# Performance work log

Hardware: AMD Instinct MI355X
Metric: run time of the kernel (lower is better)

Reference implementation:

```python
import jax, jax.numpy as jnp
import numpy as np

B, C, G = 2, 256, 32
SPATIAL = (16, 16, 16)
EPS = 1e-5


def setup_inputs() -> dict:
    key = jax.random.key(0)
    ks = jax.random.split(key, 11)
    s = 1.0 / np.sqrt(C)
    x = jax.random.normal(ks[0], (B, C) + SPATIAL, dtype=jnp.float32)
    mk = lambda k: jax.random.normal(k, (C, C), dtype=jnp.float32) * s
    return {
        "x": x,
        "Wq": mk(ks[1]), "bq": jnp.zeros((C,), jnp.float32),
        "Wk": mk(ks[2]), "bk": jnp.zeros((C,), jnp.float32),
        "Wv": mk(ks[3]), "bv": jnp.zeros((C,), jnp.float32),
        "Wo": mk(ks[4]), "bo": jnp.zeros((C,), jnp.float32),
        "gamma": jnp.ones((C,), jnp.float32),
        "beta": jnp.zeros((C,), jnp.float32),
    }


def reference(x, Wq, bq, Wk, bk, Wv, bv, Wo, bo, gamma, beta):
    b, c = x.shape[0], x.shape[1]
    xf = x.reshape(b, c, -1)  # [B, C, N]

    def proj1x1(inp, W, bias):
        return jnp.einsum('oc,bcn->bon', W, inp) + bias[None, :, None]

    q = proj1x1(xf, Wq, bq)
    k = proj1x1(xf, Wk, bk)
    v = proj1x1(xf, Wv, bv)

    # qk[b, n, m] = sum_c q[b, c, n] * k[b, c, m]   (no 1/sqrt(C) scale, as in source)
    scores = jnp.einsum('bcn,bcm->bnm', q, k)
    w = jax.nn.softmax(scores, axis=-1)
    # h[b, c, n] = sum_m v[b, c, m] * w[b, n, m]
    h = jnp.einsum('bcm,bnm->bcn', v, w)
    h = proj1x1(h, Wo, bo)

    y = xf + h  # residual

    # GroupNorm over (channels-in-group, spatial)
    yg = y.reshape(b, G, c // G, -1)
    mu = jnp.mean(yg, axis=(2, 3), keepdims=True)
    var = jnp.var(yg, axis=(2, 3), keepdims=True)
    yn = ((yg - mu) * jax.lax.rsqrt(var + EPS)).reshape(b, c, -1)
    yn = yn * gamma[None, :, None] + beta[None, :, None]

    out = yn * jax.nn.sigmoid(yn)  # SiLU
    return out.reshape(x.shape)
```

## Files before the change

kernel.cpp:

```cpp
#include <hip/hip_runtime.h>
#include <hip/hip_bf16.h>

typedef _Float16 f16;
typedef __attribute__((ext_vector_type(4))) _Float16 f16x4;
typedef __attribute__((ext_vector_type(8))) _Float16 f16x8;
typedef __attribute__((ext_vector_type(4))) float f32x4;

#define CD 256
#define ND 4096
#define GD 32
#define KVB 32

__device__ __forceinline__ void gl_lds16(const f16* g, f16* l) {
    __builtin_amdgcn_global_load_lds(
        (const __attribute__((address_space(1))) unsigned int*)g,
        (__attribute__((address_space(3))) unsigned int*)l,
        16, 0, 0);
}

__global__ __launch_bounds__(256)
void k_proj_qkv(const float* __restrict__ x,
                const float* __restrict__ Wq, const float* __restrict__ bq,
                const float* __restrict__ Wk, const float* __restrict__ bk,
                const float* __restrict__ Wv, const float* __restrict__ bv,
                f16* __restrict__ Qt, f16* __restrict__ Kt, f16* __restrict__ Vb)
{
    __shared__ f16 As[64][40];
    __shared__ f16 Bs[64][40];
    __shared__ f16 Ts[64][72];

    const int t  = threadIdx.x;
    const int n0 = blockIdx.x * 64;
    const int o0 = blockIdx.y * 64;
    const int p  = blockIdx.z % 3;
    const int bb = blockIdx.z / 3;

    const float* W    = (p == 0) ? Wq : (p == 1) ? Wk : Wv;
    const float* bias = (p == 0) ? bq : (p == 1) ? bk : bv;

    const int w  = t >> 6;
    const int l  = t & 63;
    const int lr = l & 15;
    const int lg = l >> 4;
    const int wo = (w >> 1) * 32;
    const int wn = (w & 1) * 32;

    const int sl = t & 63;
    const int k8 = (t >> 6) * 8;

    f32x4 acc[2][2] = {};

    for (int ck = 0; ck < CD; ck += 32) {
        __syncthreads();
        {
            const float* s = W + (size_t)(o0 + sl) * CD + ck + k8;
            f16x8 v;
#pragma unroll
            for (int u = 0; u < 8; ++u) v[u] = (f16)s[u];
            *(f16x8*)&As[sl][k8] = v;
        }
        {
            const float* s = x + ((size_t)bb * CD + ck + k8) * ND + n0 + sl;
            f16x8 v;
#pragma unroll
            for (int u = 0; u < 8; ++u) v[u] = (f16)s[(size_t)u * ND];
            *(f16x8*)&Bs[sl][k8] = v;
        }
        __syncthreads();
        f16x8 a0 = *(const f16x8*)&As[wo + lr][lg * 8];
        f16x8 a1 = *(const f16x8*)&As[wo + 16 + lr][lg * 8];
        f16x8 b0 = *(const f16x8*)&Bs[wn + lr][lg * 8];
        f16x8 b1 = *(const f16x8*)&Bs[wn + 16 + lr][lg * 8];
        acc[0][0] = __builtin_amdgcn_mfma_f32_16x16x32_f16(a0, b0, acc[0][0], 0, 0, 0);
        acc[0][1] = __builtin_amdgcn_mfma_f32_16x16x32_f16(a0, b1, acc[0][1], 0, 0, 0);
        acc[1][0] = __builtin_amdgcn_mfma_f32_16x16x32_f16(a1, b0, acc[1][0], 0, 0, 0);
        acc[1][1] = __builtin_amdgcn_mfma_f32_16x16x32_f16(a1, b1, acc[1][1], 0, 0, 0);
    }

    if (p < 2) {
        __syncthreads();
#pragma unroll
        for (int so = 0; so < 2; ++so)
#pragma unroll
            for (int r = 0; r < 4; ++r) {
                int orow  = wo + so * 16 + lg * 4 + r;
                float bv_ = bias[o0 + orow];
#pragma unroll
                for (int sn = 0; sn < 2; ++sn)
                    Ts[orow][wn + sn * 16 + lr] = (f16)(acc[so][sn][r] + bv_);
            }
        __syncthreads();
        f16* dst = (p == 0) ? Qt : Kt;
        int n  = t >> 2;
        int o8 = (t & 3) * 16;
        f16 tmp[16];
#pragma unroll
        for (int u = 0; u < 16; ++u) tmp[u] = Ts[o8 + u][n];
        f16* g = dst + ((size_t)bb * ND + n0 + n) * CD + o0 + o8;
        *(f16x8*)g       = *(f16x8*)&tmp[0];
        *(f16x8*)(g + 8) = *(f16x8*)&tmp[8];
    } else {
#pragma unroll
        for (int so = 0; so < 2; ++so)
#pragma unroll
            for (int r = 0; r < 4; ++r) {
                int orow  = wo + so * 16 + lg * 4 + r;
                float bv_ = bias[o0 + orow];
#pragma unroll
                for (int sn = 0; sn < 2; ++sn) {
                    int ncol = wn + sn * 16 + lr;
                    Vb[((size_t)bb * CD + o0 + orow) * ND + n0 + ncol] =
                        (f16)(acc[so][sn][r] + bv_);
                }
            }
    }
}

template<int KSN>
__global__ __launch_bounds__(256, 2)
void k_attn(const f16* __restrict__ Qt, const f16* __restrict__ Kt,
            const f16* __restrict__ Vb, f16* __restrict__ Op,
            float* __restrict__ ml)
{
    __shared__ f16 Ks[2][32 * 256];
    __shared__ f16 Vs[2][256 * 32];
    __shared__ f16 Pl[4][32][40];

    const int t  = threadIdx.x;
    const int w  = t >> 6;
    const int l  = t & 63;
    const int lr = l & 15;
    const int lg = l >> 4;
    const int ks = blockIdx.y;
    const int bb = blockIdx.z;
    const int q0 = blockIdx.x * 128 + w * 32;

    f16x8 qf[2][8];
#pragma unroll
    for (int qs = 0; qs < 2; ++qs)
#pragma unroll
        for (int kc = 0; kc < 8; ++kc)
            qf[qs][kc] = *(const f16x8*)(Qt + ((size_t)bb * ND + q0 + qs * 16 + lr) * CD + kc * 32 + lg * 8);

    f32x4 oacc[2][16] = {};
    float row_m[2] = { -3.0e38f, -3.0e38f };
    float row_l[2] = { 0.f, 0.f };

    const int kv0 = ks * (ND / KSN);
    const f16* ktb = Kt + (size_t)bb * ND * CD;
    const f16* vbb = Vb + (size_t)bb * CD * ND;

    int koff[4], voff[4];
#pragma unroll
    for (int j = 0; j < 4; ++j) {
        int v   = (w * 4 + j) * 64 + l;
        int row = v >> 5;
        int ch  = (v & 31) ^ (row & 7);
        koff[j] = row * CD + ch * 8;
        int c   = v >> 2;
        int u   = (v & 3) ^ ((c >> 1) & 3);
        voff[j] = c * ND + u * 8;
    }

    auto stage = [&](int m0, int bi) {
#pragma unroll
        for (int j = 0; j < 4; ++j)
            gl_lds16(ktb + (size_t)m0 * CD + koff[j], &Ks[bi][(w * 4 + j) * 512]);
#pragma unroll
        for (int j = 0; j < 4; ++j)
            gl_lds16(vbb + m0 + voff[j], &Vs[bi][(w * 4 + j) * 512]);
    };

    stage(kv0, 0);
    __syncthreads();

    const int NIT = (ND / KSN) / KVB;
    for (int it = 0; it < NIT; ++it) {
        const int bi = it & 1;
        if (it + 1 < NIT) stage(kv0 + (it + 1) * KVB, bi ^ 1);

        f32x4 s[2][2] = {};
        __builtin_amdgcn_s_setprio(1);
#pragma unroll
        for (int kc = 0; kc < 8; ++kc) {
            int chs = ((kc * 4 + lg) ^ (lr & 7)) * 8;
            f16x8 k0 = *(const f16x8*)&Ks[bi][(lr) * 256 + chs];
            f16x8 k1 = *(const f16x8*)&Ks[bi][(16 + lr) * 256 + chs];
            s[0][0] = __builtin_amdgcn_mfma_f32_16x16x32_f16(k0, qf[0][kc], s[0][0], 0, 0, 0);
            s[1][0] = __builtin_amdgcn_mfma_f32_16x16x32_f16(k1, qf[0][kc], s[1][0], 0, 0, 0);
            s[0][1] = __builtin_amdgcn_mfma_f32_16x16x32_f16(k0, qf[1][kc], s[0][1], 0, 0, 0);
            s[1][1] = __builtin_amdgcn_mfma_f32_16x16x32_f16(k1, qf[1][kc], s[1][1], 0, 0, 0);
        }
        __builtin_amdgcn_s_setprio(0);

#pragma unroll
        for (int qs = 0; qs < 2; ++qs) {
            float pm = fmaxf(
                fmaxf(fmaxf(s[0][qs][0], s[0][qs][1]), fmaxf(s[0][qs][2], s[0][qs][3])),
                fmaxf(fmaxf(s[1][qs][0], s[1][qs][1]), fmaxf(s[1][qs][2], s[1][qs][3])));
            pm = fmaxf(pm, __shfl_xor(pm, 16));
            pm = fmaxf(pm, __shfl_xor(pm, 32));
            float nm = fmaxf(row_m[qs], pm);
            float sc = __expf(row_m[qs] - nm);
            float p0 = __expf(s[0][qs][0] - nm);
            float p1 = __expf(s[0][qs][1] - nm);
            float p2 = __expf(s[0][qs][2] - nm);
            float p3 = __expf(s[0][qs][3] - nm);
            float p4 = __expf(s[1][qs][0] - nm);
            float p5 = __expf(s[1][qs][1] - nm);
            float p6 = __expf(s[1][qs][2] - nm);
            float p7 = __expf(s[1][qs][3] - nm);
            float ps = ((p0 + p1) + (p2 + p3)) + ((p4 + p5) + (p6 + p7));
            ps += __shfl_xor(ps, 16);
            ps += __shfl_xor(ps, 32);
            bool chg = nm > row_m[qs];
            row_l[qs] = row_l[qs] * sc + ps;
            row_m[qs] = nm;
            if (__any(chg)) {
#pragma unroll
                for (int ct = 0; ct < 16; ++ct) {
                    oacc[qs][ct][0] *= sc; oacc[qs][ct][1] *= sc;
                    oacc[qs][ct][2] *= sc; oacc[qs][ct][3] *= sc;
                }
            }
            f16x4 pk0 = { (f16)p0, (f16)p1, (f16)p2, (f16)p3 };
            f16x4 pk1 = { (f16)p4, (f16)p5, (f16)p6, (f16)p7 };
            *(f16x4*)&Pl[w][qs * 16 + lr][lg * 4]      = pk0;
            *(f16x4*)&Pl[w][qs * 16 + lr][16 + lg * 4] = pk1;
        }

        f16x8 pf0 = *(const f16x8*)&Pl[w][lr][lg * 8];
        f16x8 pf1 = *(const f16x8*)&Pl[w][16 + lr][lg * 8];
        __builtin_amdgcn_s_setprio(1);
#pragma unroll
        for (int ct = 0; ct < 16; ++ct) {
            f16x8 vf = *(const f16x8*)&Vs[bi][(ct * 16 + lr) * 32 + ((lg ^ ((lr >> 1) & 3))) * 8];
            oacc[0][ct] = __builtin_amdgcn_mfma_f32_16x16x32_f16(vf, pf0, oacc[0][ct], 0, 0, 0);
            oacc[1][ct] = __builtin_amdgcn_mfma_f32_16x16x32_f16(vf, pf1, oacc[1][ct], 0, 0, 0);
        }
        __builtin_amdgcn_s_setprio(0);
        __syncthreads();
    }

#pragma unroll
    for (int qs = 0; qs < 2; ++qs)
#pragma unroll
        for (int ct = 0; ct < 16; ++ct)
#pragma unroll
            for (int r = 0; r < 4; ++r) {
                int cch = ct * 16 + lg * 4 + r;
                Op[(((size_t)ks * 2 + bb) * CD + cch) * ND + q0 + qs * 16 + lr] =
                    (f16)oacc[qs][ct][r];
            }
    if (lg == 0) {
#pragma unroll
        for (int qs = 0; qs < 2; ++qs) {
            int n = q0 + qs * 16 + lr;
            ml[((ks * 2 + bb) * 2 + 0) * ND + n] = row_m[qs];
            ml[((ks * 2 + bb) * 2 + 1) * ND + n] = row_l[qs];
        }
    }
}

template<int KSN>
__global__ __launch_bounds__(256)
void k_ml(const float* __restrict__ ml, float* __restrict__ wq)
{
    int i = blockIdx.x * 256 + threadIdx.x;
    int b = i / ND, n = i % ND;
    float m[KSN], lv[KSN];
#pragma unroll
    for (int ks = 0; ks < KSN; ++ks) {
        m[ks]  = ml[((ks * 2 + b) * 2 + 0) * ND + n];
        lv[ks] = ml[((ks * 2 + b) * 2 + 1) * ND + n];
    }
    float M = m[0];
#pragma unroll
    for (int ks = 1; ks < KSN; ++ks) M = fmaxf(M, m[ks]);
    float wgt[KSN], L = 0.f;
#pragma unroll
    for (int ks = 0; ks < KSN; ++ks) { wgt[ks] = __expf(m[ks] - M); L += wgt[ks] * lv[ks]; }
    float inv = 1.0f / L;
#pragma unroll
    for (int ks = 0; ks < KSN; ++ks)
        wq[(ks * 2 + b) * ND + n] = wgt[ks] * inv;
}

template<int KSN>
__global__ __launch_bounds__(256)
void k_comb(const f16* __restrict__ Op, const float* __restrict__ wq,
            f16* __restrict__ Hb)
{
    size_t i = (size_t)blockIdx.x * 256 + threadIdx.x;
    int n0 = (int)(i % (ND / 8)) * 8;
    int c  = (int)((i / (ND / 8)) % CD);
    int b  = (int)(i / ((size_t)CD * (ND / 8)));

    float acc[8] = {};
#pragma unroll
    for (int ks = 0; ks < KSN; ++ks) {
        f16x8 o = *(const f16x8*)(Op + (((size_t)ks * 2 + b) * CD + c) * ND + n0);
        const float* wp = wq + (ks * 2 + b) * ND + n0;
        float4 w0 = *(const float4*)wp;
        float4 w1 = *(const float4*)(wp + 4);
        acc[0] += w0.x * (float)o[0]; acc[1] += w0.y * (float)o[1];
        acc[2] += w0.z * (float)o[2]; acc[3] += w0.w * (float)o[3];
        acc[4] += w1.x * (float)o[4]; acc[5] += w1.y * (float)o[5];
        acc[6] += w1.z * (float)o[6]; acc[7] += w1.w * (float)o[7];
    }
    f16x8 h;
#pragma unroll
    for (int u = 0; u < 8; ++u) h[u] = (f16)acc[u];
    *(f16x8*)(Hb + ((size_t)b * CD + c) * ND + n0) = h;
}

__global__ __launch_bounds__(256)
void k_proj_o(const f16* __restrict__ Hb, const float* __restrict__ Wo,
              const float* __restrict__ bo, const float* __restrict__ x,
              float* __restrict__ Y)
{
    __shared__ f16 As[64][40];
    __shared__ f16 Bs[64][40];

    const int t  = threadIdx.x;
    const int n0 = blockIdx.x * 64;
    const int o0 = blockIdx.y * 64;
    const int bb = blockIdx.z;

    const int w  = t >> 6;
    const int l  = t & 63;
    const int lr = l & 15;
    const int lg = l >> 4;
    const int wo = (w >> 1) * 32;
    const int wn = (w & 1) * 32;

    const int sl = t & 63;
    const int k8 = (t >> 6) * 8;

    f32x4 acc[2][2] = {};

    for (int ck = 0; ck < CD; ck += 32) {
        __syncthreads();
        {
            const float* s = Wo + (size_t)(o0 + sl) * CD + ck + k8;
            f16x8 v;
#pragma unroll
            for (int u = 0; u < 8; ++u) v[u] = (f16)s[u];
            *(f16x8*)&As[sl][k8] = v;
        }
        {
            const f16* s = Hb + ((size_t)bb * CD + ck + k8) * ND + n0 + sl;
            f16x8 v;
#pragma unroll
            for (int u = 0; u < 8; ++u) v[u] = s[(size_t)u * ND];
            *(f16x8*)&Bs[sl][k8] = v;
        }
        __syncthreads();
        f16x8 a0 = *(const f16x8*)&As[wo + lr][lg * 8];
        f16x8 a1 = *(const f16x8*)&As[wo + 16 + lr][lg * 8];
        f16x8 b0 = *(const f16x8*)&Bs[wn + lr][lg * 8];
        f16x8 b1 = *(const f16x8*)&Bs[wn + 16 + lr][lg * 8];
        acc[0][0] = __builtin_amdgcn_mfma_f32_16x16x32_f16(a0, b0, acc[0][0], 0, 0, 0);
        acc[0][1] = __builtin_amdgcn_mfma_f32_16x16x32_f16(a0, b1, acc[0][1], 0, 0, 0);
        acc[1][0] = __builtin_amdgcn_mfma_f32_16x16x32_f16(a1, b0, acc[1][0], 0, 0, 0);
        acc[1][1] = __builtin_amdgcn_mfma_f32_16x16x32_f16(a1, b1, acc[1][1], 0, 0, 0);
    }

#pragma unroll
    for (int so = 0; so < 2; ++so)
#pragma unroll
        for (int r = 0; r < 4; ++r) {
            int orow  = wo + so * 16 + lg * 4 + r;
            float bv_ = bo[o0 + orow];
#pragma unroll
            for (int sn = 0; sn < 2; ++sn) {
                int ncol   = wn + sn * 16 + lr;
                size_t idx = ((size_t)bb * CD + o0 + orow) * ND + n0 + ncol;
                Y[idx] = acc[so][sn][r] + bv_ + x[idx];
            }
        }
}

__global__ __launch_bounds__(256)
void k_stats(const float* __restrict__ Y, float* __restrict__ stats)
{
    const int g = blockIdx.x, b = blockIdx.y;
    const float* base = Y + ((size_t)b * CD + g * 8) * ND;
    float s = 0.f, s2 = 0.f;
    for (int i = threadIdx.x; i < (8 * ND) / 4; i += 256) {
        float4 v = ((const float4*)base)[i];
        s  += v.x + v.y + v.z + v.w;
        s2 += v.x * v.x + v.y * v.y + v.z * v.z + v.w * v.w;
    }
#pragma unroll
    for (int m = 1; m < 64; m <<= 1) {
        s  += __shfl_xor(s, m);
        s2 += __shfl_xor(s2, m);
    }
    __shared__ float red[8];
    if ((threadIdx.x & 63) == 0) {
        red[(threadIdx.x >> 6) * 2]     = s;
        red[(threadIdx.x >> 6) * 2 + 1] = s2;
    }
    __syncthreads();
    if (threadIdx.x == 0) {
        float S  = red[0] + red[2] + red[4] + red[6];
        float S2 = red[1] + red[3] + red[5] + red[7];
        float mean = S / 32768.f;
        float var  = S2 / 32768.f - mean * mean;
        stats[(b * GD + g) * 2]     = mean;
        stats[(b * GD + g) * 2 + 1] = rsqrtf(var + 1e-5f);
    }
}

__global__ __launch_bounds__(256)
void k_norm_silu(const float* __restrict__ Y, const float* __restrict__ stats,
                 const float* __restrict__ gamma, const float* __restrict__ beta,
                 float* __restrict__ out)
{
    size_t i4 = (size_t)blockIdx.x * 256 + threadIdx.x;
    int c = (int)((i4 / (ND / 4)) % CD);
    int b = (int)(i4 / ((size_t)CD * (ND / 4)));
    float mean = stats[(b * GD + c / 8) * 2];
    float rstd = stats[(b * GD + c / 8) * 2 + 1];
    float ga = gamma[c], be = beta[c];
    float4 v = ((const float4*)Y)[i4];
    float in[4] = { v.x, v.y, v.z, v.w };
    float ob[4];
#pragma unroll
    for (int u = 0; u < 4; ++u) {
        float yn = (in[u] - mean) * rstd * ga + be;
        float sg = 1.0f / (1.0f + __expf(-yn));
        ob[u] = yn * sg;
    }
    *(float4*)(out + i4 * 4) = *(float4*)ob;
}

extern "C" void kernel_launch(void* const* d_in, const int* in_sizes, int n_in,
                              void* d_out, int out_size, void* d_ws, size_t ws_size,
                              hipStream_t stream)
{
    const float* x     = (const float*)d_in[0];
    const float* Wq    = (const float*)d_in[1];
    const float* bq    = (const float*)d_in[2];
    const float* Wk    = (const float*)d_in[3];
    const float* bk    = (const float*)d_in[4];
    const float* Wv    = (const float*)d_in[5];
    const float* bv    = (const float*)d_in[6];
    const float* Wo    = (const float*)d_in[7];
    const float* bo    = (const float*)d_in[8];
    const float* gamma = (const float*)d_in[9];
    const float* beta  = (const float*)d_in[10];

    char* ws = (char*)d_ws;
    f16* Qt = (f16*)(ws);
    f16* Kt = (f16*)(ws + (4u << 20));
    f16* Vb = (f16*)(ws + (8u << 20));
    f16* Hb = (f16*)(ws + (12u << 20));
    f16* Op = (f16*)(ws + (16u << 20));
    float* Y = (float*)(ws + (16u << 20));

    const bool big = ws_size >= (50ull << 20);

    k_proj_qkv<<<dim3(64, 4, 6), 256, 0, stream>>>(x, Wq, bq, Wk, bk, Wv, bv, Qt, Kt, Vb);

    if (big) {
        constexpr int KSN = 8;
        float* ml    = (float*)(ws + (48u << 20));
        float* wq    = (float*)(ws + (48u << 20) + (768u << 10));
        float* stats = (float*)(ws + (49u << 20) + (512u << 10));
        k_attn<KSN><<<dim3(32, KSN, 2), 256, 0, stream>>>(Qt, Kt, Vb, Op, ml);
        k_ml<KSN><<<dim3((2 * ND) / 256), 256, 0, stream>>>(ml, wq);
        k_comb<KSN><<<dim3((2 * CD * ND / 8) / 256), 256, 0, stream>>>(Op, wq, Hb);
        k_proj_o<<<dim3(64, 4, 2), 256, 0, stream>>>(Hb, Wo, bo, x, Y);
        k_stats<<<dim3(32, 2), 256, 0, stream>>>(Y, stats);
        k_norm_silu<<<2048, 256, 0, stream>>>(Y, stats, gamma, beta, (float*)d_out);
    } else {
        constexpr int KSN = 4;
        float* ml    = (float*)(ws + (32u << 20));
        float* wq    = (float*)(ws + (32u << 20) + (512u << 10));
        float* stats = (float*)(ws + (33u << 20));
        k_attn<KSN><<<dim3(32, KSN, 2), 256, 0, stream>>>(Qt, Kt, Vb, Op, ml);
        k_ml<KSN><<<dim3((2 * ND) / 256), 256, 0, stream>>>(ml, wq);
        k_comb<KSN><<<dim3((2 * CD * ND / 8) / 256), 256, 0, stream>>>(Op, wq, Hb);
        k_proj_o<<<dim3(64, 4, 2), 256, 0, stream>>>(Hb, Wo, bo, x, Y);
        k_stats<<<dim3(32, 2), 256, 0, stream>>>(Y, stats);
        k_norm_silu<<<2048, 256, 0, stream>>>(Y, stats, gamma, beta, (float*)d_out);
    }
}
```

Measured before the change: 121.3 us.

## Fuse QKV projections per block and split attention into 8 waves of 16 rows

The QKV projection kernel now computes Q, K and V in one block, sharing the x tile staged in LDS, instead of launching separate blocks per projection. The attention kernel moves to 512 threads, with each wave owning 16 query rows instead of 32. This halves the per-wave accumulator and Q-fragment registers and raises the occupancy target to 4 blocks. The trade-off is lower MFMA reuse of each K/V fragment per wave, more LDS traffic per FLOP, and fewer projection blocks with more registers each.

```diff
diff --git a/kernel.cpp b/kernel.cpp
--- a/kernel.cpp
+++ b/kernel.cpp
@@ -25,18 +25,17 @@
                 const float* __restrict__ Wv, const float* __restrict__ bv,
                 f16* __restrict__ Qt, f16* __restrict__ Kt, f16* __restrict__ Vb)
 {
-    __shared__ f16 As[64][40];
+    __shared__ f16 As[3][64][40];
     __shared__ f16 Bs[64][40];
     __shared__ f16 Ts[64][72];
 
     const int t  = threadIdx.x;
     const int n0 = blockIdx.x * 64;
     const int o0 = blockIdx.y * 64;
-    const int p  = blockIdx.z % 3;
-    const int bb = blockIdx.z / 3;
-
-    const float* W    = (p == 0) ? Wq : (p == 1) ? Wk : Wv;
-    const float* bias = (p == 0) ? bq : (p == 1) ? bk : bv;
+    const int bb = blockIdx.z;
+
+    const float* Ws[3] = { Wq, Wk, Wv };
+    const float* bs[3] = { bq, bk, bv };
 
     const int w  = t >> 6;
     const int l  = t & 63;
@@ -48,16 +47,17 @@
     const int sl = t & 63;
     const int k8 = (t >> 6) * 8;
 
-    f32x4 acc[2][2] = {};
+    f32x4 acc[3][2][2] = {};
 
     for (int ck = 0; ck < CD; ck += 32) {
         __syncthreads();
-        {
-            const float* s = W + (size_t)(o0 + sl) * CD + ck + k8;
+#pragma unroll
+        for (int p = 0; p < 3; ++p) {
+            const float* s = Ws[p] + (size_t)(o0 + sl) * CD + ck + k8;
             f16x8 v;
 #pragma unroll
             for (int u = 0; u < 8; ++u) v[u] = (f16)s[u];
-            *(f16x8*)&As[sl][k8] = v;
+            *(f16x8*)&As[p][sl][k8] = v;
         }
         {
             const float* s = x + ((size_t)bb * CD + ck + k8) * ND + n0 + sl;
@@ -67,27 +67,31 @@
             *(f16x8*)&Bs[sl][k8] = v;
         }
         __syncthreads();
-        f16x8 a0 = *(const f16x8*)&As[wo + lr][lg * 8];
-        f16x8 a1 = *(const f16x8*)&As[wo + 16 + lr][lg * 8];
         f16x8 b0 = *(const f16x8*)&Bs[wn + lr][lg * 8];
         f16x8 b1 = *(const f16x8*)&Bs[wn + 16 + lr][lg * 8];
-        acc[0][0] = __builtin_amdgcn_mfma_f32_16x16x32_f16(a0, b0, acc[0][0], 0, 0, 0);
-        acc[0][1] = __builtin_amdgcn_mfma_f32_16x16x32_f16(a0, b1, acc[0][1], 0, 0, 0);
-        acc[1][0] = __builtin_amdgcn_mfma_f32_16x16x32_f16(a1, b0, acc[1][0], 0, 0, 0);
-        acc[1][1] = __builtin_amdgcn_mfma_f32_16x16x32_f16(a1, b1, acc[1][1], 0, 0, 0);
-    }
-
-    if (p < 2) {
+#pragma unroll
+        for (int p = 0; p < 3; ++p) {
+            f16x8 a0 = *(const f16x8*)&As[p][wo + lr][lg * 8];
+            f16x8 a1 = *(const f16x8*)&As[p][wo + 16 + lr][lg * 8];
+            acc[p][0][0] = __builtin_amdgcn_mfma_f32_16x16x32_f16(a0, b0, acc[p][0][0], 0, 0, 0);
+            acc[p][0][1] = __builtin_amdgcn_mfma_f32_16x16x32_f16(a0, b1, acc[p][0][1], 0, 0, 0);
+            acc[p][1][0] = __builtin_amdgcn_mfma_f32_16x16x32_f16(a1, b0, acc[p][1][0], 0, 0, 0);
+            acc[p][1][1] = __builtin_amdgcn_mfma_f32_16x16x32_f16(a1, b1, acc[p][1][1], 0, 0, 0);
+        }
+    }
+
+#pragma unroll
+    for (int p = 0; p < 2; ++p) {
         __syncthreads();
 #pragma unroll
         for (int so = 0; so < 2; ++so)
 #pragma unroll
             for (int r = 0; r < 4; ++r) {
                 int orow  = wo + so * 16 + lg * 4 + r;
-                float bv_ = bias[o0 + orow];
+                float bv_ = bs[p][o0 + orow];
 #pragma unroll
                 for (int sn = 0; sn < 2; ++sn)
-                    Ts[orow][wn + sn * 16 + lr] = (f16)(acc[so][sn][r] + bv_);
+                    Ts[orow][wn + sn * 16 + lr] = (f16)(acc[p][so][sn][r] + bv_);
             }
         __syncthreads();
         f16* dst = (p == 0) ? Qt : Kt;
@@ -99,32 +103,31 @@
         f16* g = dst + ((size_t)bb * ND + n0 + n) * CD + o0 + o8;
         *(f16x8*)g       = *(f16x8*)&tmp[0];
         *(f16x8*)(g + 8) = *(f16x8*)&tmp[8];
-    } else {
-#pragma unroll
-        for (int so = 0; so < 2; ++so)
-#pragma unroll
-            for (int r = 0; r < 4; ++r) {
-                int orow  = wo + so * 16 + lg * 4 + r;
-                float bv_ = bias[o0 + orow];
-#pragma unroll
-                for (int sn = 0; sn < 2; ++sn) {
-                    int ncol = wn + sn * 16 + lr;
-                    Vb[((size_t)bb * CD + o0 + orow) * ND + n0 + ncol] =
-                        (f16)(acc[so][sn][r] + bv_);
-                }
+    }
+#pragma unroll
+    for (int so = 0; so < 2; ++so)
+#pragma unroll
+        for (int r = 0; r < 4; ++r) {
+            int orow  = wo + so * 16 + lg * 4 + r;
+            float bv_ = bv[o0 + orow];
+#pragma unroll
+            for (int sn = 0; sn < 2; ++sn) {
+                int ncol = wn + sn * 16 + lr;
+                Vb[((size_t)bb * CD + o0 + orow) * ND + n0 + ncol] =
+                    (f16)(acc[2][so][sn][r] + bv_);
             }
-    }
+        }
 }
 
 template<int KSN>
-__global__ __launch_bounds__(256, 2)
+__global__ __launch_bounds__(512, 4)
 void k_attn(const f16* __restrict__ Qt, const f16* __restrict__ Kt,
             const f16* __restrict__ Vb, f16* __restrict__ Op,
             float* __restrict__ ml)
 {
     __shared__ f16 Ks[2][32 * 256];
     __shared__ f16 Vs[2][256 * 32];
-    __shared__ f16 Pl[4][32][40];
+    __shared__ f16 Pl[8][16][36];
 
     const int t  = threadIdx.x;
     const int w  = t >> 6;
@@ -133,42 +136,39 @@
     const int lg = l >> 4;
     const int ks = blockIdx.y;
     const int bb = blockIdx.z;
-    const int q0 = blockIdx.x * 128 + w * 32;
-
-    f16x8 qf[2][8];
-#pragma unroll
-    for (int qs = 0; qs < 2; ++qs)
-#pragma unroll
-        for (int kc = 0; kc < 8; ++kc)
-            qf[qs][kc] = *(const f16x8*)(Qt + ((size_t)bb * ND + q0 + qs * 16 + lr) * CD + kc * 32 + lg * 8);
-
-    f32x4 oacc[2][16] = {};
-    float row_m[2] = { -3.0e38f, -3.0e38f };
-    float row_l[2] = { 0.f, 0.f };
+    const int q0 = blockIdx.x * 128 + w * 16;
+
+    f16x8 qf[8];
+#pragma unroll
+    for (int kc = 0; kc < 8; ++kc)
+        qf[kc] = *(const f16x8*)(Qt + ((size_t)bb * ND + q0 + lr) * CD + kc * 32 + lg * 8);
+
+    f32x4 oacc[16] = {};
+    float row_m = -3.0e38f, row_l = 0.f;
 
     const int kv0 = ks * (ND / KSN);
     const f16* ktb = Kt + (size_t)bb * ND * CD;
     const f16* vbb = Vb + (size_t)bb * CD * ND;
 
-    int koff[4], voff[4];
-#pragma unroll
-    for (int j = 0; j < 4; ++j) {
-        int v   = (w * 4 + j) * 64 + l;
-        int row = v >> 5;
-        int ch  = (v & 31) ^ (row & 7);
-        koff[j] = row * CD + ch * 8;
-        int c   = v >> 2;
-        int u   = (v & 3) ^ ((c >> 1) & 3);
-        voff[j] = c * ND + u * 8;
+    int koff[2], voff[2];
+#pragma unroll
+    for (int j = 0; j < 2; ++j) {
+        int cidx = (w * 2 + j) * 64 + l;
+        int krow = cidx >> 5;
+        int kch  = (cidx & 31) ^ (krow & 7);
+        koff[j]  = krow * CD + kch * 8;
+        int vc   = cidx >> 2;
+        int vu   = (cidx & 3) ^ ((vc >> 1) & 3);
+        voff[j]  = vc * ND + vu * 8;
     }
 
     auto stage = [&](int m0, int bi) {
 #pragma unroll
-        for (int j = 0; j < 4; ++j)
-            gl_lds16(ktb + (size_t)m0 * CD + koff[j], &Ks[bi][(w * 4 + j) * 512]);
-#pragma unroll
-        for (int j = 0; j < 4; ++j)
-            gl_lds16(vbb + m0 + voff[j], &Vs[bi][(w * 4 + j) * 512]);
+        for (int j = 0; j < 2; ++j)
+            gl_lds16(ktb + (size_t)m0 * CD + koff[j], &Ks[bi][(w * 2 + j) * 512]);
+#pragma unroll
+        for (int j = 0; j < 2; ++j)
+            gl_lds16(vbb + m0 + voff[j], &Vs[bi][(w * 2 + j) * 512]);
     };
 
     stage(kv0, 0);
@@ -179,86 +179,75 @@
         const int bi = it & 1;
         if (it + 1 < NIT) stage(kv0 + (it + 1) * KVB, bi ^ 1);
 
-        f32x4 s[2][2] = {};
+        f32x4 s0 = {}, s1 = {};
         __builtin_amdgcn_s_setprio(1);
 #pragma unroll
         for (int kc = 0; kc < 8; ++kc) {
             int chs = ((kc * 4 + lg) ^ (lr & 7)) * 8;
             f16x8 k0 = *(const f16x8*)&Ks[bi][(lr) * 256 + chs];
             f16x8 k1 = *(const f16x8*)&Ks[bi][(16 + lr) * 256 + chs];
-            s[0][0] = __builtin_amdgcn_mfma_f32_16x16x32_f16(k0, qf[0][kc], s[0][0], 0, 0, 0);
-            s[1][0] = __builtin_amdgcn_mfma_f32_16x16x32_f16(k1, qf[0][kc], s[1][0], 0, 0, 0);
-            s[0][1] = __builtin_amdgcn_mfma_f32_16x16x32_f16(k0, qf[1][kc], s[0][1], 0, 0, 0);
-            s[1][1] = __builtin_amdgcn_mfma_f32_16x16x32_f16(k1, qf[1][kc], s[1][1], 0, 0, 0);
+            s0 = __builtin_amdgcn_mfma_f32_16x16x32_f16(k0, qf[kc], s0, 0, 0, 0);
+            s1 = __builtin_amdgcn_mfma_f32_16x16x32_f16(k1, qf[kc], s1, 0, 0, 0);
         }
         __builtin_amdgcn_s_setprio(0);
 
-#pragma unroll
-        for (int qs = 0; qs < 2; ++qs) {
+        {
             float pm = fmaxf(
-                fmaxf(fmaxf(s[0][qs][0], s[0][qs][1]), fmaxf(s[0][qs][2], s[0][qs][3])),
-                fmaxf(fmaxf(s[1][qs][0], s[1][qs][1]), fmaxf(s[1][qs][2], s[1][qs][3])));
+                fmaxf(fmaxf(s0[0], s0[1]), fmaxf(s0[2], s0[3])),
+                fmaxf(fmaxf(s1[0], s1[1]), fmaxf(s1[2], s1[3])));
             pm = fmaxf(pm, __shfl_xor(pm, 16));
             pm = fmaxf(pm, __shfl_xor(pm, 32));
-            float nm = fmaxf(row_m[qs], pm);
-            float sc = __expf(row_m[qs] - nm);
-            float p0 = __expf(s[0][qs][0] - nm);
-            float p1 = __expf(s[0][qs][1] - nm);
-            float p2 = __expf(s[0][qs][2] - nm);
-            float p3 = __expf(s[0][qs][3] - nm);
-            float p4 = __expf(s[1][qs][0] - nm);
-            float p5 = __expf(s[1][qs][1] - nm);
-            float p6 = __expf(s[1][qs][2] - nm);
-            float p7 = __expf(s[1][qs][3] - nm);
+            float nm = fmaxf(row_m, pm);
+            float sc = __expf(row_m - nm);
+            float p0 = __expf(s0[0] - nm);
+            float p1 = __expf(s0[1] - nm);
+            float p2 = __expf(s0[2] - nm);
+            float p3 = __expf(s0[3] - nm);
+            float p4 = __expf(s1[0] - nm);
+            float p5 = __expf(s1[1] - nm);
+            float p6 = __expf(s1[2] - nm);
+            float p7 = __expf(s1[3] - nm);
             float ps = ((p0 + p1) + (p2 + p3)) + ((p4 + p5) + (p6 + p7));
             ps += __shfl_xor(ps, 16);
             ps += __shfl_xor(ps, 32);
-            bool chg = nm > row_m[qs];
-            row_l[qs] = row_l[qs] * sc + ps;
-            row_m[qs] = nm;
+            bool chg = nm > row_m;
+            row_l = row_l * sc + ps;
+            row_m = nm;
             if (__any(chg)) {
 #pragma unroll
                 for (int ct = 0; ct < 16; ++ct) {
-                    oacc[qs][ct][0] *= sc; oacc[qs][ct][1] *= sc;
-                    oacc[qs][ct][2] *= sc; oacc[qs][ct][3] *= sc;
+                    oacc[ct][0] *= sc; oacc[ct][1] *= sc;
+                    oacc[ct][2] *= sc; oacc[ct][3] *= sc;
                 }
             }
             f16x4 pk0 = { (f16)p0, (f16)p1, (f16)p2, (f16)p3 };
             f16x4 pk1 = { (f16)p4, (f16)p5, (f16)p6, (f16)p7 };
-            *(f16x4*)&Pl[w][qs * 16 + lr][lg * 4]      = pk0;
-            *(f16x4*)&Pl[w][qs * 16 + lr][16 + lg * 4] = pk1;
-        }
-
-        f16x8 pf0 = *(const f16x8*)&Pl[w][lr][lg * 8];
-        f16x8 pf1 = *(const f16x8*)&Pl[w][16 + lr][lg * 8];
+            *(f16x4*)&Pl[w][lr][lg * 4]      = pk0;
+            *(f16x4*)&Pl[w][lr][16 + lg * 4] = pk1;
+        }
+
+        f16x8 pf = *(const f16x8*)&Pl[w][lr][lg * 8];
         __builtin_amdgcn_s_setprio(1);
 #pragma unroll
         for (int ct = 0; ct < 16; ++ct) {
             f16x8 vf = *(const f16x8*)&Vs[bi][(ct * 16 + lr) * 32 + ((lg ^ ((lr >> 1) & 3))) * 8];
-            oacc[0][ct] = __builtin_amdgcn_mfma_f32_16x16x32_f16(vf, pf0, oacc[0][ct], 0, 0, 0);
-            oacc[1][ct] = __builtin_amdgcn_mfma_f32_16x16x32_f16(vf, pf1, oacc[1][ct], 0, 0, 0);
+            oacc[ct] = __builtin_amdgcn_mfma_f32_16x16x32_f16(vf, pf, oacc[ct], 0, 0, 0);
         }
         __builtin_amdgcn_s_setprio(0);
         __syncthreads();
     }
 
 #pragma unroll
-    for (int qs = 0; qs < 2; ++qs)
-#pragma unroll
-        for (int ct = 0; ct < 16; ++ct)
-#pragma unroll
-            for (int r = 0; r < 4; ++r) {
-                int cch = ct * 16 + lg * 4 + r;
-                Op[(((size_t)ks * 2 + bb) * CD + cch) * ND + q0 + qs * 16 + lr] =
-                    (f16)oacc[qs][ct][r];
-            }
+    for (int ct = 0; ct < 16; ++ct)
+#pragma unroll
+        for (int r = 0; r < 4; ++r) {
+            int cch = ct * 16 + lg * 4 + r;
+            Op[(((size_t)ks * 2 + bb) * CD + cch) * ND + q0 + lr] = (f16)oacc[ct][r];
+        }
     if (lg == 0) {
-#pragma unroll
-        for (int qs = 0; qs < 2; ++qs) {
-            int n = q0 + qs * 16 + lr;
-            ml[((ks * 2 + bb) * 2 + 0) * ND + n] = row_m[qs];
-            ml[((ks * 2 + bb) * 2 + 1) * ND + n] = row_l[qs];
-        }
+        int n = q0 + lr;
+        ml[((ks * 2 + bb) * 2 + 0) * ND + n] = row_m;
+        ml[((ks * 2 + bb) * 2 + 1) * ND + n] = row_l;
     }
 }
 
@@ -462,14 +451,14 @@
 
     const bool big = ws_size >= (50ull << 20);
 
-    k_proj_qkv<<<dim3(64, 4, 6), 256, 0, stream>>>(x, Wq, bq, Wk, bk, Wv, bv, Qt, Kt, Vb);
+    k_proj_qkv<<<dim3(64, 4, 2), 256, 0, stream>>>(x, Wq, bq, Wk, bk, Wv, bv, Qt, Kt, Vb);
 
     if (big) {
         constexpr int KSN = 8;
         float* ml    = (float*)(ws + (48u << 20));
         float* wq    = (float*)(ws + (48u << 20) + (768u << 10));
         float* stats = (float*)(ws + (49u << 20) + (512u << 10));
-        k_attn<KSN><<<dim3(32, KSN, 2), 256, 0, stream>>>(Qt, Kt, Vb, Op, ml);
+        k_attn<KSN><<<dim3(32, KSN, 2), 512, 0, stream>>>(Qt, Kt, Vb, Op, ml);
         k_ml<KSN><<<dim3((2 * ND) / 256), 256, 0, stream>>>(ml, wq);
         k_comb<KSN><<<dim3((2 * CD * ND / 8) / 256), 256, 0, stream>>>(Op, wq, Hb);
         k_proj_o<<<dim3(64, 4, 2), 256, 0, stream>>>(Hb, Wo, bo, x, Y);
@@ -480,7 +469,7 @@
         float* ml    = (float*)(ws + (32u << 20));
         float* wq    = (float*)(ws + (32u << 20) + (512u << 10));
         float* stats = (float*)(ws + (33u << 20));
-        k_attn<KSN><<<dim3(32, KSN, 2), 256, 0, stream>>>(Qt, Kt, Vb, Op, ml);
+        k_attn<KSN><<<dim3(32, KSN, 2), 512, 0, stream>>>(Qt, Kt, Vb, Op, ml);
         k_ml<KSN><<<dim3((2 * ND) / 256), 256, 0, stream>>>(ml, wq);
         k_comb<KSN><<<dim3((2 * CD * ND / 8) / 256), 256, 0, stream>>>(Op, wq, Hb);
         k_proj_o<<<dim3(64, 4, 2), 256, 0, stream>>>(Hb, Wo, bo, x, Y);
```

After: 124.3 us. 1.03x slower.
